# Kernel tuning notes

Hardware: AMD Instinct MI355X
Metric: run time of the kernel (lower is better)

## Reference

```python
import jax, jax.numpy as jnp
import numpy as np

H = 64  # hidden size
T = 11  # unrolled timesteps


def setup_inputs() -> dict:
    key = jax.random.key(0)
    ks = jax.random.split(key, 8)
    B, V, E = 65536, 50000, 100
    return {
        "sent": jax.random.randint(ks[0], (B, T), 0, V, dtype=jnp.int32),
        "emb_W": jax.random.normal(ks[1], (V, E), jnp.float32) * 0.05,
        "W_ih": jax.random.normal(ks[2], (4 * H, E), jnp.float32) * 0.05,
        "W_hh": jax.random.normal(ks[3], (4 * H, H), jnp.float32) * 0.05,
        "b_ih": jax.random.normal(ks[4], (4 * H,), jnp.float32) * 0.05,
        "b_hh": jax.random.normal(ks[5], (4 * H,), jnp.float32) * 0.05,
        "fc_W": jax.random.normal(ks[6], (14, H), jnp.float32) * 0.05,
        "fc_b": jax.random.normal(ks[7], (14,), jnp.float32) * 0.05,
    }


def _lstm_cell(x, h, c, W_ih, W_hh, b_ih, b_hh):
    # gates order in torch LSTMCell: i, f, g, o
    gates = x @ W_ih.T + b_ih + h @ W_hh.T + b_hh  # [B, 4H]
    i, f, g, o = jnp.split(gates, 4, axis=-1)
    c_new = jax.nn.sigmoid(f) * c + jax.nn.sigmoid(i) * jnp.tanh(g)
    h_new = jax.nn.sigmoid(o) * jnp.tanh(c_new)
    return h_new, c_new


def reference(sent, emb_W, W_ih, W_hh, b_ih, b_hh, fc_W, fc_b):
    embed = emb_W[sent]  # [B, T, E]
    B = embed.shape[0]
    h0 = jnp.zeros((B, H), embed.dtype)
    c0 = jnp.zeros((B, H), embed.dtype)
    xs = jnp.swapaxes(embed[:, :T, :], 0, 1)  # [T, B, E]

    def step(carry, x):
        h, c = carry
        h, c = _lstm_cell(x, h, c, W_ih, W_hh, b_ih, b_hh)
        return (h, c), None

    (h_last, _), _ = jax.lax.scan(step, (h0, c0), xs)
    logits = h_last @ fc_W.T + fc_b  # [B, 14]
    return jax.nn.log_softmax(logits, axis=-1)
```

## Files before the change

kernel.cpp:

```cpp
#include <hip/hip_runtime.h>
#include <hip/hip_bf16.h>

#define T_STEPS 11
#define E_DIM   100
#define XSL     2048
#define NDMA    (2 * T_STEPS)

typedef int   i32x4   __attribute__((ext_vector_type(4)));
typedef int   i32x8   __attribute__((ext_vector_type(8)));
typedef float f32x4   __attribute__((ext_vector_type(4)));
typedef _Float16 h16x2 __attribute__((ext_vector_type(2)));
typedef _Float16 h16x4 __attribute__((ext_vector_type(4)));
typedef _Float16 h16x8 __attribute__((ext_vector_type(8)));

typedef __attribute__((address_space(1))) const unsigned int g_as1;
typedef __attribute__((address_space(3))) unsigned int l_as3;

__device__ __forceinline__ h16x2 spl2(float v) {
    _Float16 h = (_Float16)v;
    return (h16x2){h, h};
}
__device__ __forceinline__ h16x2 pk2(float a, float b) {
    return __builtin_bit_cast(h16x2, __builtin_amdgcn_cvt_pkrtz(a, b));
}
__device__ __forceinline__ unsigned char f2fp8(float f) {
    return (unsigned char)(__builtin_amdgcn_cvt_pk_fp8_f32(f, 0.f, 0, false) & 0xff);
}
__device__ __forceinline__ long long ll_lo(i32x4 v) {
    return ((long long)(unsigned)v[1] << 32) | (unsigned)v[0];
}
__device__ __forceinline__ long long ll_hi(i32x4 v) {
    return ((long long)(unsigned)v[3] << 32) | (unsigned)v[2];
}

__device__ __forceinline__ h16x2 tanh5(h16x2 x) {
    h16x2 x2 = x * x;
    h16x2 p = x2 * spl2(0.13333333f) + spl2(-0.33333333f);
    p = x2 * p + spl2(1.0f);
    return x * p;
}
__device__ __forceinline__ h16x2 tanh7(h16x2 x) {
    h16x2 x2 = x * x;
    h16x2 p = x2 * spl2(-0.05396825f) + spl2(0.13333333f);
    p = x2 * p + spl2(-0.33333333f);
    p = x2 * p + spl2(1.0f);
    return x * p;
}
__device__ __forceinline__ h16x2 sig3(h16x2 x) {
    h16x2 x2 = x * x;
    h16x2 p = x2 * spl2(-0.020833334f) + spl2(0.25f);
    return x * p + spl2(0.5f);
}

__global__ void pack_all(const float* __restrict__ emb,
                         const float* __restrict__ W_ih, const float* __restrict__ W_hh,
                         const float* __restrict__ b_ih, const float* __restrict__ b_hh,
                         unsigned char* __restrict__ embp8, unsigned char* __restrict__ Wx8,
                         unsigned char* __restrict__ Wh8, float* __restrict__ biasf, int V)
{
    int b = blockIdx.x;
    int tid = threadIdx.x;
    if (b < 128) {
        int id = b * 256 + tid;
        int n = id >> 7, k = id & 127;
        float v = (k < E_DIM) ? W_ih[n * E_DIM + k] : 0.f;
        int mt = n >> 4;
        int lane = (n & 15) | ((k >> 5) << 4);
        Wx8[(mt * 64 + lane) * 32 + (k & 31)] = f2fp8(v);
    } else if (b < 192) {
        int id = (b - 128) * 256 + tid;
        int n = id >> 6, k = id & 63;
        int kt = k >> 5;
        int lane = (n & 15) | (((k & 31) >> 3) << 4);
        Wh8[((kt * 16 + (n >> 4)) * 64 + lane) * 8 + (k & 7)] = f2fp8(W_hh[n * 64 + k]);
    } else if (b == 192) {
        biasf[tid] = b_ih[tid] + b_hh[tid];
    } else {
        int id = (b - 193) * 256 + tid;
        if (id >= V * 8) return;
        int row = id >> 3;
        int c8 = id & 7;
        const float* xr = emb + (size_t)row * E_DIM;
        float v[16];
        #pragma unroll
        for (int w = 0; w < 16; ++w) {
            int k = c8 * 16 + w;
            v[w] = (k < E_DIM) ? xr[k] : 0.f;
        }
        int4 o;
        int* op = &o.x;
        #pragma unroll
        for (int w = 0; w < 4; ++w) {
            int d = __builtin_amdgcn_cvt_pk_fp8_f32(v[w*4+0], v[w*4+1], 0, false);
            d = __builtin_amdgcn_cvt_pk_fp8_f32(v[w*4+2], v[w*4+3], d, true);
            op[w] = d;
        }
        *reinterpret_cast<int4*>(embp8 + (size_t)row * 128 + c8 * 16) = o;
    }
}

template<int PACKED>
__global__ __launch_bounds__(256, 4)
void lstm_fused(const int* __restrict__ sent,
                const float* __restrict__ emb, const unsigned char* __restrict__ embp8,
                const unsigned char* __restrict__ Wx8, const unsigned char* __restrict__ Wh8,
                const float* __restrict__ biasf,
                const float* __restrict__ fc_W, const float* __restrict__ fc_b,
                float* __restrict__ out)
{
    __shared__ unsigned char xlds[T_STEPS * XSL];
    __shared__ unsigned char hlds[2][1024];
    __shared__ float biaslds[256];
    __shared__ short hscr[16 * 68];
    const int tid  = threadIdx.x;
    const int wv   = tid >> 6;
    const int lane = tid & 63;
    const int r    = lane & 15;
    const int q    = lane >> 4;
    const int b0   = blockIdx.x * 16;

    for (int d = wv; d < NDMA; d += 4) {
        int sl = d >> 1, half = d & 1;
        int c  = half * 4 + (lane >> 4);
        int rr = lane & 15;
        int idx = sent[(b0 + rr) * T_STEPS + sl];
        if (PACKED) {
            const unsigned char* src = embp8 + (size_t)idx * 128 + c * 16;
            __builtin_amdgcn_global_load_lds(
                (g_as1*)src, (l_as3*)&xlds[sl * XSL + half * 1024], 16, 0, 0);
        } else {
            const float* xr = emb + (size_t)idx * E_DIM;
            float v[16];
            #pragma unroll
            for (int w = 0; w < 16; ++w) {
                int k = c * 16 + w;
                v[w] = (k < E_DIM) ? xr[k] : 0.f;
            }
            int4 o;
            int* op = &o.x;
            #pragma unroll
            for (int w = 0; w < 4; ++w) {
                int dd = __builtin_amdgcn_cvt_pk_fp8_f32(v[w*4+0], v[w*4+1], 0, false);
                dd = __builtin_amdgcn_cvt_pk_fp8_f32(v[w*4+2], v[w*4+3], dd, true);
                op[w] = dd;
            }
            *reinterpret_cast<int4*>(&xlds[sl * XSL + (c * 16 + rr) * 16]) = o;
        }
    }

    i32x8 wx[4];
    #pragma unroll
    for (int g = 0; g < 4; ++g)
        wx[g] = *reinterpret_cast<const i32x8*>(
            Wx8 + ((g * 4 + wv) * 64 + lane) * 32);
    long long wh[2][4];
    #pragma unroll
    for (int kt = 0; kt < 2; ++kt)
        #pragma unroll
        for (int g = 0; g < 4; ++g)
            wh[kt][g] = *reinterpret_cast<const long long*>(
                Wh8 + ((kt * 16 + g * 4 + wv) * 64 + lane) * 8);
    #pragma unroll
    for (int g = 0; g < 4; ++g)
        asm volatile("" : "+v"(wx[g]));
    #pragma unroll
    for (int kt = 0; kt < 2; ++kt)
        #pragma unroll
        for (int g = 0; g < 4; ++g)
            asm volatile("" : "+v"(wh[kt][g]));

    biaslds[tid] = biasf[tid];
    reinterpret_cast<int*>(&hlds[0][0])[tid] = 0;

    __builtin_amdgcn_s_waitcnt(0);
    __syncthreads();

    auto acc_bias_x = [&](int sl, f32x4* acc) {
        #pragma unroll
        for (int g = 0; g < 4; ++g)
            acc[g] = *reinterpret_cast<const f32x4*>(
                &biaslds[(g * 4 + wv) * 16 + q * 4]);
        i32x4 lo = *reinterpret_cast<const i32x4*>(
            &xlds[sl * XSL + ((2 * q) * 16 + r) * 16]);
        i32x4 hi = *reinterpret_cast<const i32x4*>(
            &xlds[sl * XSL + ((2 * q + 1) * 16 + r) * 16]);
        i32x8 bx = { lo[0], lo[1], lo[2], lo[3], hi[0], hi[1], hi[2], hi[3] };
        #pragma unroll
        for (int g = 0; g < 4; ++g)
            acc[g] = __builtin_amdgcn_mfma_scale_f32_16x16x128_f8f6f4(
                wx[g], bx, acc[g], 0, 0, 0, 127, 0, 127);
    };

    h16x2 c01 = spl2(0.f), c23 = spl2(0.f);
    f32x4 acc[4];
    acc_bias_x(0, acc);

    const int hq  = (wv & 1) * 2 + (q >> 1);
    const int hoff = (hq * 16 + r) * 16 + (wv >> 1) * 8 + (q & 1) * 4;

    #pragma unroll
    for (int t = 0; t < T_STEPS; ++t) {
        __builtin_amdgcn_s_setprio(1);
        i32x4 hv = *reinterpret_cast<const i32x4*>(&hlds[t & 1][(q * 16 + r) * 16]);
        long long bh0 = ll_lo(hv), bh1 = ll_hi(hv);
        #pragma unroll
        for (int g = 0; g < 4; ++g)
            acc[g] = __builtin_amdgcn_mfma_f32_16x16x32_fp8_fp8(wh[0][g], bh0, acc[g], 0, 0, 0);
        #pragma unroll
        for (int g = 0; g < 4; ++g)
            acc[g] = __builtin_amdgcn_mfma_f32_16x16x32_fp8_fp8(wh[1][g], bh1, acc[g], 0, 0, 0);

        h16x2 gi0 = pk2(acc[0][0], acc[0][1]), gi1 = pk2(acc[0][2], acc[0][3]);
        h16x2 gf0 = pk2(acc[1][0], acc[1][1]), gf1 = pk2(acc[1][2], acc[1][3]);
        h16x2 gg0 = pk2(acc[2][0], acc[2][1]), gg1 = pk2(acc[2][2], acc[2][3]);
        h16x2 go0 = pk2(acc[3][0], acc[3][1]), go1 = pk2(acc[3][2], acc[3][3]);
        c01 = sig3(gf0) * c01 + sig3(gi0) * tanh5(gg0);
        c23 = sig3(gf1) * c23 + sig3(gi1) * tanh5(gg1);
        h16x2 h01 = sig3(go0) * tanh7(c01);
        h16x2 h23 = sig3(go1) * tanh7(c23);

        int hw = __builtin_amdgcn_cvt_pk_fp8_f32((float)h01[0], (float)h01[1], 0, false);
        hw = __builtin_amdgcn_cvt_pk_fp8_f32((float)h23[0], (float)h23[1], hw, true);
        *reinterpret_cast<int*>(&hlds[(t + 1) & 1][hoff]) = hw;
        __builtin_amdgcn_s_setprio(0);

        if (t == T_STEPS - 1) {
            h16x4 hn = { h01[0], h01[1], h23[0], h23[1] };
            *reinterpret_cast<h16x4*>(&hscr[r * 68 + wv * 16 + q * 4]) = hn;
        }

        if (t + 1 < T_STEPS) acc_bias_x(t + 1, acc);

        __syncthreads();
    }

    const int row_local = wv * 4 + q;
    const int cls = r;
    const int brow = b0 + row_local;
    float s = (cls < 14) ? fc_b[cls] : 0.f;
    const float* wrow = fc_W + ((cls < 14) ? cls : 0) * 64;
    #pragma unroll
    for (int ch = 0; ch < 8; ++ch) {
        h16x8 hv8 = *reinterpret_cast<const h16x8*>(&hscr[row_local * 68 + ch * 8]);
        #pragma unroll
        for (int j = 0; j < 8; ++j)
            s = fmaf((float)hv8[j], wrow[ch * 8 + j], s);
    }
    float lg = (cls < 14) ? s : -1e30f;
    float mx = lg;
    mx = fmaxf(mx, __shfl_xor(mx, 1));
    mx = fmaxf(mx, __shfl_xor(mx, 2));
    mx = fmaxf(mx, __shfl_xor(mx, 4));
    mx = fmaxf(mx, __shfl_xor(mx, 8));
    float se = __expf(lg - mx);
    se += __shfl_xor(se, 1);
    se += __shfl_xor(se, 2);
    se += __shfl_xor(se, 4);
    se += __shfl_xor(se, 8);
    float lse = mx + __logf(se);
    if (cls < 14) out[(size_t)brow * 14 + cls] = lg - lse;
}

extern "C" void kernel_launch(void* const* d_in, const int* in_sizes, int n_in,
                              void* d_out, int out_size, void* d_ws, size_t ws_size,
                              hipStream_t stream)
{
    const int*   sent = (const int*)d_in[0];
    const float* emb  = (const float*)d_in[1];
    const float* W_ih = (const float*)d_in[2];
    const float* W_hh = (const float*)d_in[3];
    const float* b_ih = (const float*)d_in[4];
    const float* b_hh = (const float*)d_in[5];
    const float* fc_W = (const float*)d_in[6];
    const float* fc_b = (const float*)d_in[7];
    float* out = (float*)d_out;

    const int B = in_sizes[0] / T_STEPS;
    const int V = in_sizes[1] / E_DIM;
    const size_t emb_bytes = (size_t)V * 128;
    const size_t need = emb_bytes + 32768 + 16384 + 1024;
    const bool packed = ws_size >= need;

    unsigned char* embp8 = (unsigned char*)d_ws;
    unsigned char* Wx8   = embp8 + emb_bytes;
    unsigned char* Wh8   = Wx8 + 32768;
    float*         biasf = (float*)(Wh8 + 16384);
    if (!packed) {
        Wx8   = (unsigned char*)d_ws;
        Wh8   = Wx8 + 32768;
        biasf = (float*)(Wh8 + 16384);
        embp8 = nullptr;
    }

    const int grid = B / 16;
    if (packed) {
        int pgrid = 193 + (V * 8 + 255) / 256;
        pack_all<<<pgrid, 256, 0, stream>>>(emb, W_ih, W_hh, b_ih, b_hh,
                                            embp8, Wx8, Wh8, biasf, V);
        lstm_fused<1><<<grid, 256, 0, stream>>>(sent, emb, embp8, Wx8, Wh8,
                                                biasf, fc_W, fc_b, out);
    } else {
        pack_all<<<193, 256, 0, stream>>>(emb, W_ih, W_hh, b_ih, b_hh,
                                          nullptr, Wx8, Wh8, biasf, 0);
        lstm_fused<0><<<grid, 256, 0, stream>>>(sent, emb, nullptr, Wx8, Wh8,
                                                biasf, fc_W, fc_b, out);
    }
}
```

Measured before the change: 151.1 us.

## Process two 16-row batch groups per block to interleave independent recurrences

Each block now handles 32 batch rows as two independent 16-row groups. Their MFMAs and gate math are interleaved within each timestep, so one group's work can hide the other's latency while the per-wave weight registers are reused across both. The grid is halved and LDS per block roughly doubles, so launch bounds drop to 3 blocks per CU. The cost is lower occupancy and more registers per thread, and with half as many blocks the work may spread less evenly across CUs.

```diff
diff --git a/kernel.cpp b/kernel.cpp
--- a/kernel.cpp
+++ b/kernel.cpp
@@ -4,7 +4,7 @@
 #define T_STEPS 11
 #define E_DIM   100
 #define XSL     2048
-#define NDMA    (2 * T_STEPS)
+#define NDMA    (4 * T_STEPS)
 
 typedef int   i32x4   __attribute__((ext_vector_type(4)));
 typedef int   i32x8   __attribute__((ext_vector_type(8)));
@@ -100,7 +100,7 @@
 }
 
 template<int PACKED>
-__global__ __launch_bounds__(256, 4)
+__global__ __launch_bounds__(256, 3)
 void lstm_fused(const int* __restrict__ sent,
                 const float* __restrict__ emb, const unsigned char* __restrict__ embp8,
                 const unsigned char* __restrict__ Wx8, const unsigned char* __restrict__ Wh8,
@@ -108,26 +108,29 @@
                 const float* __restrict__ fc_W, const float* __restrict__ fc_b,
                 float* __restrict__ out)
 {
-    __shared__ unsigned char xlds[T_STEPS * XSL];
-    __shared__ unsigned char hlds[2][1024];
+    __shared__ unsigned char xlds[2][T_STEPS * XSL];
+    __shared__ unsigned char hlds[2][2][1024];
     __shared__ float biaslds[256];
-    __shared__ short hscr[16 * 68];
+    __shared__ short hscr[2][16 * 68];
     const int tid  = threadIdx.x;
     const int wv   = tid >> 6;
     const int lane = tid & 63;
     const int r    = lane & 15;
     const int q    = lane >> 4;
-    const int b0   = blockIdx.x * 16;
-
+    const int b0   = blockIdx.x * 32;
+
+    #pragma unroll
     for (int d = wv; d < NDMA; d += 4) {
-        int sl = d >> 1, half = d & 1;
+        int grp = d >= 22;
+        int dd  = d - grp * 22;
+        int sl = dd >> 1, half = dd & 1;
         int c  = half * 4 + (lane >> 4);
         int rr = lane & 15;
-        int idx = sent[(b0 + rr) * T_STEPS + sl];
+        int idx = sent[(b0 + grp * 16 + rr) * T_STEPS + sl];
         if (PACKED) {
             const unsigned char* src = embp8 + (size_t)idx * 128 + c * 16;
             __builtin_amdgcn_global_load_lds(
-                (g_as1*)src, (l_as3*)&xlds[sl * XSL + half * 1024], 16, 0, 0);
+                (g_as1*)src, (l_as3*)&xlds[grp][sl * XSL + half * 1024], 16, 0, 0);
         } else {
             const float* xr = emb + (size_t)idx * E_DIM;
             float v[16];
@@ -140,11 +143,11 @@
             int* op = &o.x;
             #pragma unroll
             for (int w = 0; w < 4; ++w) {
-                int dd = __builtin_amdgcn_cvt_pk_fp8_f32(v[w*4+0], v[w*4+1], 0, false);
-                dd = __builtin_amdgcn_cvt_pk_fp8_f32(v[w*4+2], v[w*4+3], dd, true);
-                op[w] = dd;
+                int e = __builtin_amdgcn_cvt_pk_fp8_f32(v[w*4+0], v[w*4+1], 0, false);
+                e = __builtin_amdgcn_cvt_pk_fp8_f32(v[w*4+2], v[w*4+3], e, true);
+                op[w] = e;
             }
-            *reinterpret_cast<int4*>(&xlds[sl * XSL + (c * 16 + rr) * 16]) = o;
+            *reinterpret_cast<int4*>(&xlds[grp][sl * XSL + (c * 16 + rr) * 16]) = o;
         }
     }
 
@@ -170,20 +173,21 @@
             asm volatile("" : "+v"(wh[kt][g]));
 
     biaslds[tid] = biasf[tid];
-    reinterpret_cast<int*>(&hlds[0][0])[tid] = 0;
+    reinterpret_cast<int*>(&hlds[0][0][0])[tid] = 0;
+    reinterpret_cast<int*>(&hlds[0][0][0])[256 + tid] = 0;
 
     __builtin_amdgcn_s_waitcnt(0);
     __syncthreads();
 
-    auto acc_bias_x = [&](int sl, f32x4* acc) {
+    auto acc_bias_x = [&](int grp, int sl, f32x4* acc) {
         #pragma unroll
         for (int g = 0; g < 4; ++g)
             acc[g] = *reinterpret_cast<const f32x4*>(
                 &biaslds[(g * 4 + wv) * 16 + q * 4]);
         i32x4 lo = *reinterpret_cast<const i32x4*>(
-            &xlds[sl * XSL + ((2 * q) * 16 + r) * 16]);
+            &xlds[grp][sl * XSL + ((2 * q) * 16 + r) * 16]);
         i32x4 hi = *reinterpret_cast<const i32x4*>(
-            &xlds[sl * XSL + ((2 * q + 1) * 16 + r) * 16]);
+            &xlds[grp][sl * XSL + ((2 * q + 1) * 16 + r) * 16]);
         i32x8 bx = { lo[0], lo[1], lo[2], lo[3], hi[0], hi[1], hi[2], hi[3] };
         #pragma unroll
         for (int g = 0; g < 4; ++g)
@@ -191,9 +195,11 @@
                 wx[g], bx, acc[g], 0, 0, 0, 127, 0, 127);
     };
 
-    h16x2 c01 = spl2(0.f), c23 = spl2(0.f);
-    f32x4 acc[4];
-    acc_bias_x(0, acc);
+    h16x2 c01a = spl2(0.f), c23a = spl2(0.f);
+    h16x2 c01b = spl2(0.f), c23b = spl2(0.f);
+    f32x4 acc0[4], acc1[4];
+    acc_bias_x(0, 0, acc0);
+    acc_bias_x(1, 0, acc1);
 
     const int hq  = (wv & 1) * 2 + (q >> 1);
     const int hoff = (hq * 16 + r) * 16 + (wv >> 1) * 8 + (q & 1) * 4;
@@ -201,64 +207,94 @@
     #pragma unroll
     for (int t = 0; t < T_STEPS; ++t) {
         __builtin_amdgcn_s_setprio(1);
-        i32x4 hv = *reinterpret_cast<const i32x4*>(&hlds[t & 1][(q * 16 + r) * 16]);
-        long long bh0 = ll_lo(hv), bh1 = ll_hi(hv);
-        #pragma unroll
-        for (int g = 0; g < 4; ++g)
-            acc[g] = __builtin_amdgcn_mfma_f32_16x16x32_fp8_fp8(wh[0][g], bh0, acc[g], 0, 0, 0);
-        #pragma unroll
-        for (int g = 0; g < 4; ++g)
-            acc[g] = __builtin_amdgcn_mfma_f32_16x16x32_fp8_fp8(wh[1][g], bh1, acc[g], 0, 0, 0);
-
-        h16x2 gi0 = pk2(acc[0][0], acc[0][1]), gi1 = pk2(acc[0][2], acc[0][3]);
-        h16x2 gf0 = pk2(acc[1][0], acc[1][1]), gf1 = pk2(acc[1][2], acc[1][3]);
-        h16x2 gg0 = pk2(acc[2][0], acc[2][1]), gg1 = pk2(acc[2][2], acc[2][3]);
-        h16x2 go0 = pk2(acc[3][0], acc[3][1]), go1 = pk2(acc[3][2], acc[3][3]);
-        c01 = sig3(gf0) * c01 + sig3(gi0) * tanh5(gg0);
-        c23 = sig3(gf1) * c23 + sig3(gi1) * tanh5(gg1);
-        h16x2 h01 = sig3(go0) * tanh7(c01);
-        h16x2 h23 = sig3(go1) * tanh7(c23);
-
-        int hw = __builtin_amdgcn_cvt_pk_fp8_f32((float)h01[0], (float)h01[1], 0, false);
-        hw = __builtin_amdgcn_cvt_pk_fp8_f32((float)h23[0], (float)h23[1], hw, true);
-        *reinterpret_cast<int*>(&hlds[(t + 1) & 1][hoff]) = hw;
+        i32x4 hv0 = *reinterpret_cast<const i32x4*>(&hlds[t & 1][0][(q * 16 + r) * 16]);
+        i32x4 hv1 = *reinterpret_cast<const i32x4*>(&hlds[t & 1][1][(q * 16 + r) * 16]);
+        long long b00 = ll_lo(hv0), b01 = ll_hi(hv0);
+        long long b10 = ll_lo(hv1), b11 = ll_hi(hv1);
+        #pragma unroll
+        for (int g = 0; g < 4; ++g) {
+            acc0[g] = __builtin_amdgcn_mfma_f32_16x16x32_fp8_fp8(wh[0][g], b00, acc0[g], 0, 0, 0);
+            acc1[g] = __builtin_amdgcn_mfma_f32_16x16x32_fp8_fp8(wh[0][g], b10, acc1[g], 0, 0, 0);
+        }
+        #pragma unroll
+        for (int g = 0; g < 4; ++g) {
+            acc0[g] = __builtin_amdgcn_mfma_f32_16x16x32_fp8_fp8(wh[1][g], b01, acc0[g], 0, 0, 0);
+            acc1[g] = __builtin_amdgcn_mfma_f32_16x16x32_fp8_fp8(wh[1][g], b11, acc1[g], 0, 0, 0);
+        }
+
+        {
+            h16x2 gi0 = pk2(acc0[0][0], acc0[0][1]), gi1 = pk2(acc0[0][2], acc0[0][3]);
+            h16x2 gf0 = pk2(acc0[1][0], acc0[1][1]), gf1 = pk2(acc0[1][2], acc0[1][3]);
+            h16x2 gg0 = pk2(acc0[2][0], acc0[2][1]), gg1 = pk2(acc0[2][2], acc0[2][3]);
+            h16x2 go0 = pk2(acc0[3][0], acc0[3][1]), go1 = pk2(acc0[3][2], acc0[3][3]);
+            c01a = sig3(gf0) * c01a + sig3(gi0) * tanh5(gg0);
+            c23a = sig3(gf1) * c23a + sig3(gi1) * tanh5(gg1);
+            h16x2 h01 = sig3(go0) * tanh7(c01a);
+            h16x2 h23 = sig3(go1) * tanh7(c23a);
+            int hw = __builtin_amdgcn_cvt_pk_fp8_f32((float)h01[0], (float)h01[1], 0, false);
+            hw = __builtin_amdgcn_cvt_pk_fp8_f32((float)h23[0], (float)h23[1], hw, true);
+            *reinterpret_cast<int*>(&hlds[(t + 1) & 1][0][hoff]) = hw;
+            if (t == T_STEPS - 1) {
+                h16x4 hn = { h01[0], h01[1], h23[0], h23[1] };
+                *reinterpret_cast<h16x4*>(&hscr[0][r * 68 + wv * 16 + q * 4]) = hn;
+            }
+        }
+        {
+            h16x2 gi0 = pk2(acc1[0][0], acc1[0][1]), gi1 = pk2(acc1[0][2], acc1[0][3]);
+            h16x2 gf0 = pk2(acc1[1][0], acc1[1][1]), gf1 = pk2(acc1[1][2], acc1[1][3]);
+            h16x2 gg0 = pk2(acc1[2][0], acc1[2][1]), gg1 = pk2(acc1[2][2], acc1[2][3]);
+            h16x2 go0 = pk2(acc1[3][0], acc1[3][1]), go1 = pk2(acc1[3][2], acc1[3][3]);
+            c01b = sig3(gf0) * c01b + sig3(gi0) * tanh5(gg0);
+            c23b = sig3(gf1) * c23b + sig3(gi1) * tanh5(gg1);
+            h16x2 h01 = sig3(go0) * tanh7(c01b);
+            h16x2 h23 = sig3(go1) * tanh7(c23b);
+            int hw = __builtin_amdgcn_cvt_pk_fp8_f32((float)h01[0], (float)h01[1], 0, false);
+            hw = __builtin_amdgcn_cvt_pk_fp8_f32((float)h23[0], (float)h23[1], hw, true);
+            *reinterpret_cast<int*>(&hlds[(t + 1) & 1][1][hoff]) = hw;
+            if (t == T_STEPS - 1) {
+                h16x4 hn = { h01[0], h01[1], h23[0], h23[1] };
+                *reinterpret_cast<h16x4*>(&hscr[1][r * 68 + wv * 16 + q * 4]) = hn;
+            }
+        }
         __builtin_amdgcn_s_setprio(0);
 
-        if (t == T_STEPS - 1) {
-            h16x4 hn = { h01[0], h01[1], h23[0], h23[1] };
-            *reinterpret_cast<h16x4*>(&hscr[r * 68 + wv * 16 + q * 4]) = hn;
-        }
-
-        if (t + 1 < T_STEPS) acc_bias_x(t + 1, acc);
+        if (t + 1 < T_STEPS) {
+            acc_bias_x(0, t + 1, acc0);
+            acc_bias_x(1, t + 1, acc1);
+        }
 
         __syncthreads();
     }
 
     const int row_local = wv * 4 + q;
     const int cls = r;
-    const int brow = b0 + row_local;
-    float s = (cls < 14) ? fc_b[cls] : 0.f;
     const float* wrow = fc_W + ((cls < 14) ? cls : 0) * 64;
-    #pragma unroll
-    for (int ch = 0; ch < 8; ++ch) {
-        h16x8 hv8 = *reinterpret_cast<const h16x8*>(&hscr[row_local * 68 + ch * 8]);
-        #pragma unroll
-        for (int j = 0; j < 8; ++j)
-            s = fmaf((float)hv8[j], wrow[ch * 8 + j], s);
-    }
-    float lg = (cls < 14) ? s : -1e30f;
-    float mx = lg;
-    mx = fmaxf(mx, __shfl_xor(mx, 1));
-    mx = fmaxf(mx, __shfl_xor(mx, 2));
-    mx = fmaxf(mx, __shfl_xor(mx, 4));
-    mx = fmaxf(mx, __shfl_xor(mx, 8));
-    float se = __expf(lg - mx);
-    se += __shfl_xor(se, 1);
-    se += __shfl_xor(se, 2);
-    se += __shfl_xor(se, 4);
-    se += __shfl_xor(se, 8);
-    float lse = mx + __logf(se);
-    if (cls < 14) out[(size_t)brow * 14 + cls] = lg - lse;
+    float fb = (cls < 14) ? fc_b[cls] : 0.f;
+    #pragma unroll
+    for (int grp = 0; grp < 2; ++grp) {
+        const int brow = b0 + grp * 16 + row_local;
+        float s = fb;
+        #pragma unroll
+        for (int ch = 0; ch < 8; ++ch) {
+            h16x8 hv8 = *reinterpret_cast<const h16x8*>(&hscr[grp][row_local * 68 + ch * 8]);
+            #pragma unroll
+            for (int j = 0; j < 8; ++j)
+                s = fmaf((float)hv8[j], wrow[ch * 8 + j], s);
+        }
+        float lg = (cls < 14) ? s : -1e30f;
+        float mx = lg;
+        mx = fmaxf(mx, __shfl_xor(mx, 1));
+        mx = fmaxf(mx, __shfl_xor(mx, 2));
+        mx = fmaxf(mx, __shfl_xor(mx, 4));
+        mx = fmaxf(mx, __shfl_xor(mx, 8));
+        float se = __expf(lg - mx);
+        se += __shfl_xor(se, 1);
+        se += __shfl_xor(se, 2);
+        se += __shfl_xor(se, 4);
+        se += __shfl_xor(se, 8);
+        float lse = mx + __logf(se);
+        if (cls < 14) out[(size_t)brow * 14 + cls] = lg - lse;
+    }
 }
 
 extern "C" void kernel_launch(void* const* d_in, const int* in_sizes, int n_in,
@@ -292,7 +328,7 @@
         embp8 = nullptr;
     }
 
-    const int grid = B / 16;
+    const int grid = B / 32;
     if (packed) {
         int pgrid = 193 + (V * 8 + 255) / 256;
         pack_all<<<pgrid, 256, 0, stream>>>(emb, W_ih, W_hh, b_ih, b_hh,
```

Measured after the change: 166.4 us. 1.1x slower.
